# Optimization experiments

Measured on AMD Instinct MI355X. Metric: run time of the kernel, lower is better.

## Reference

```python
import jax, jax.numpy as jnp
import numpy as np

N = 50000      # nodes
E = 400000     # edges (before self-loops)
IN = 256       # in_dim
H = 4          # heads in layer 1
C = 64         # h_dim (per-head channels, layer 1)
OUT = 16       # out_dim (layer 2, 1 head)
NEG_SLOPE = 0.2


def gatv2_layer(x, src, dst, Wl, bl, Wr, br, att, bias, heads, ch, concat, num_nodes):
    # x: [N, F]; src/dst: [E']; Wl/Wr: [F, heads*ch]; att: [heads, ch]
    xl = (x @ Wl + bl).reshape(num_nodes, heads, ch)  # source transform
    xr = (x @ Wr + br).reshape(num_nodes, heads, ch)  # target transform
    m = xl[src] + xr[dst]                              # [E', H, C] gather
    e = jnp.sum(jax.nn.leaky_relu(m, NEG_SLOPE) * att, axis=-1)  # [E', H]
    # segment softmax over incoming edges of each dst node (self-loops ensure non-empty)
    emax = jax.ops.segment_max(e, dst, num_segments=num_nodes)   # [N, H]
    ee = jnp.exp(e - emax[dst])
    denom = jax.ops.segment_sum(ee, dst, num_segments=num_nodes)  # [N, H]
    alpha = ee / (denom[dst] + 1e-16)                              # [E', H]
    out = jax.ops.segment_sum(alpha[..., None] * xl[src], dst, num_segments=num_nodes)  # [N,H,C]
    if concat:
        out = out.reshape(num_nodes, heads * ch)
    else:
        out = out.mean(axis=1)
    return out + bias


def setup_inputs() -> dict:
    key = jax.random.key(0)
    ks = jax.random.split(key, 16)
    s = 0.05
    inp = {
        "x": jax.random.normal(ks[0], (N, IN), jnp.float32),
        "edge_index": jax.random.randint(ks[1], (2, E), 0, N),
        # layer 1 params (in_dim -> heads*h_dim)
        "Wl1": jax.random.normal(ks[2], (IN, H * C), jnp.float32) * s,
        "bl1": jnp.zeros((H * C,), jnp.float32),
        "Wr1": jax.random.normal(ks[3], (IN, H * C), jnp.float32) * s,
        "br1": jnp.zeros((H * C,), jnp.float32),
        "att1": jax.random.normal(ks[4], (H, C), jnp.float32) * s,
        "bias1": jnp.zeros((H * C,), jnp.float32),
        # layer 2 params (heads*h_dim -> out_dim, 1 head)
        "Wl2": jax.random.normal(ks[5], (H * C, OUT), jnp.float32) * s,
        "bl2": jnp.zeros((OUT,), jnp.float32),
        "Wr2": jax.random.normal(ks[6], (H * C, OUT), jnp.float32) * s,
        "br2": jnp.zeros((OUT,), jnp.float32),
        "att2": jax.random.normal(ks[7], (1, OUT), jnp.float32) * s,
        "bias2": jnp.zeros((OUT,), jnp.float32),
    }
    return inp


def reference(x, edge_index, Wl1, bl1, Wr1, br1, att1, bias1, Wl2, bl2, Wr2, br2, att2, bias2):
    # add self loops (PyG GATv2Conv default add_self_loops=True)
    loop = jnp.arange(N, dtype=edge_index.dtype)
    src = jnp.concatenate([edge_index[0], loop])
    dst = jnp.concatenate([edge_index[1], loop])
    h = gatv2_layer(x, src, dst, Wl1, bl1, Wr1, br1, att1, bias1, H, C, True, N)
    h = jnp.tanh(h)
    o = gatv2_layer(h, src, dst, Wl2, bl2, Wr2, br2, att2, bias2, 1, OUT, False, N)
    return o, jax.nn.log_softmax(o, axis=1)
```

## Files before the change

kernel.cpp:

```cpp
#include <hip/hip_runtime.h>

typedef __bf16 bfv8 __attribute__((ext_vector_type(8)));
typedef float f32x4 __attribute__((ext_vector_type(4)));
typedef short shortv8 __attribute__((ext_vector_type(8)));
typedef unsigned short usv8 __attribute__((ext_vector_type(8)));

__device__ __forceinline__ float b2f(unsigned short u) {
  unsigned int v = ((unsigned int)u) << 16;
  float f;
  __builtin_memcpy(&f, &v, 4);
  return f;
}
__device__ __forceinline__ unsigned short f2b(float f) {
  unsigned int u;
  __builtin_memcpy(&u, &f, 4);
  u += 0x7fffu + ((u >> 16) & 1u);
  return (unsigned short)(u >> 16);
}

__global__ void probe_kernel(const unsigned short* __restrict__ x, int* __restrict__ flag) {
  int lane = threadIdx.x;
  int cnt = 0;
  for (int i = lane; i < 4096; i += 64) {
    unsigned int e = (x[i] >> 7) & 0xffu;
    if (e >= 0x86u) cnt++;
  }
#pragma unroll
  for (int off = 1; off < 64; off <<= 1) cnt += __shfl_xor(cnt, off, 64);
  if (lane == 0) *flag = (cnt > 100) ? 1 : 0;
}

__global__ __launch_bounds__(256) void conv_x_kernel(const void* __restrict__ x,
                                                     unsigned short* __restrict__ dst,
                                                     const int* __restrict__ flagp, int n) {
  int i = (blockIdx.x * 256 + threadIdx.x) * 4;
  if (i >= n) return;
  if (*flagp) {
    float4 f = *reinterpret_cast<const float4*>((const float*)x + i);
    ushort4 o;
    o.x = f2b(f.x); o.y = f2b(f.y); o.z = f2b(f.z); o.w = f2b(f.w);
    *reinterpret_cast<ushort4*>(dst + i) = o;
  } else {
    *reinterpret_cast<ushort4*>(dst + i) =
        *reinterpret_cast<const ushort4*>((const unsigned short*)x + i);
  }
}

#define P_TOT 140352
__global__ __launch_bounds__(256) void conv_params_kernel(
    const void* p0, const void* p1, const void* p2, const void* p3,
    const void* p4, const void* p5, const void* p6, const void* p7,
    const void* p8, const void* p9, const void* p10, const void* p11,
    unsigned short* __restrict__ dst, const int* __restrict__ flagp) {
  int i = blockIdx.x * 256 + threadIdx.x;
  if (i >= P_TOT) return;
  const int offs[13] = {0, 65536, 65792, 131328, 131584, 131840, 132096,
                        136192, 136208, 140304, 140320, 140336, P_TOT};
  const void* ptrs[12] = {p0, p1, p2, p3, p4, p5, p6, p7, p8, p9, p10, p11};
  int flag = *flagp;
  int t = 0;
  while (i >= offs[t + 1]) t++;
  int local = i - offs[t];
  unsigned short v;
  if (flag) v = f2b(((const float*)ptrs[t])[local]);
  else v = ((const unsigned short*)ptrs[t])[local];
  dst[i] = v;
}

__global__ __launch_bounds__(256) void transpose_w_kernel(
    const unsigned short* __restrict__ Pc,
    unsigned short* __restrict__ WT1, unsigned short* __restrict__ WT2) {
  int idx = blockIdx.x * 256 + threadIdx.x;
  if (idx < 512 * 256) {
    int n = idx >> 8, k = idx & 255;
    WT1[idx] = (n < 256) ? Pc[0 + k * 256 + n]
                         : Pc[65792 + k * 256 + (n - 256)];
  } else {
    int j = idx - 512 * 256;
    if (j < 32 * 256) {
      int n = j >> 8, k = j & 255;
      WT2[j] = (n < 16) ? Pc[132096 + k * 16 + n]
                        : Pc[136208 + k * 16 + (n - 16)];
    }
  }
}

__global__ __launch_bounds__(256) void gemm1_kernel(
    const unsigned short* __restrict__ X,
    const unsigned short* __restrict__ WT,
    const unsigned short* __restrict__ bl, const unsigned short* __restrict__ br,
    unsigned short* __restrict__ C, int M) {
  __shared__ unsigned short smem[18432];
  const int t = threadIdx.x;
  const int lane = t & 63;
  const int w = t >> 6;
  const int quad = lane >> 4;
  const int l16 = lane & 15;
  const int n_blk = blockIdx.x;
  const int m_base = blockIdx.y * 128 + (w >> 1) * 64;
  const int n_base = n_blk * 128 + (w & 1) * 64;

  const int st_row = t >> 3;
  const int st_seg = t & 7;
  const unsigned short* wt_base =
      WT + ((size_t)(n_blk * 128 + st_row)) * 256 + st_seg * 8;

  f32x4 acc[4][4];
#pragma unroll
  for (int i = 0; i < 4; i++)
#pragma unroll
    for (int j = 0; j < 4; j++) acc[i][j] = (f32x4){0.f, 0.f, 0.f, 0.f};

  shortv8 st[4];
#pragma unroll
  for (int i = 0; i < 4; i++)
    st[i] = *reinterpret_cast<const shortv8*>(wt_base + (size_t)(32 * i) * 256);
#pragma unroll
  for (int i = 0; i < 4; i++) {
    int row = st_row + 32 * i;
    *reinterpret_cast<shortv8*>(smem + row * 64 + ((st_seg ^ (row & 7)) * 8)) = st[i];
  }
  __syncthreads();

#pragma unroll
  for (int c = 0; c < 4; c++) {
    if (c < 3) {
#pragma unroll
      for (int i = 0; i < 4; i++)
        st[i] = *reinterpret_cast<const shortv8*>(wt_base + (size_t)(32 * i) * 256 +
                                                  (c + 1) * 64);
    }
    const unsigned short* bb = smem + (c & 1) * 8192;
#pragma unroll
    for (int sub = 0; sub < 2; sub++) {
      bfv8 a[4], b[4];
      int seg_r = sub * 4 + quad;
#pragma unroll
      for (int i = 0; i < 4; i++) {
        int row = m_base + 16 * i + l16;
        if (row >= M) row = M - 1;
        a[i] = *reinterpret_cast<const bfv8*>(X + (size_t)row * 256 + c * 64 + sub * 32 +
                                              quad * 8);
      }
#pragma unroll
      for (int j = 0; j < 4; j++) {
        int col = (w & 1) * 64 + 16 * j + l16;
        b[j] = *reinterpret_cast<const bfv8*>(bb + col * 64 + ((seg_r ^ (col & 7)) * 8));
      }
#pragma unroll
      for (int i = 0; i < 4; i++)
#pragma unroll
        for (int j = 0; j < 4; j++)
          acc[i][j] = __builtin_amdgcn_mfma_f32_16x16x32_bf16(a[i], b[j], acc[i][j], 0, 0, 0);
    }
    if (c < 3) {
      int buf = (c + 1) & 1;
#pragma unroll
      for (int i = 0; i < 4; i++) {
        int row = st_row + 32 * i;
        *reinterpret_cast<shortv8*>(smem + buf * 8192 + row * 64 +
                                    ((st_seg ^ (row & 7)) * 8)) = st[i];
      }
      __syncthreads();
    }
  }

  __syncthreads();
  unsigned short* lt = smem + w * 4608;
#pragma unroll
  for (int j = 0; j < 4; j++) {
    int col = n_base + 16 * j + l16;
    float bias = (col < 256) ? b2f(bl[col]) : b2f(br[col - 256]);
#pragma unroll
    for (int i = 0; i < 4; i++)
#pragma unroll
      for (int r = 0; r < 4; r++)
        lt[(16 * i + quad * 4 + r) * 72 + 16 * j + l16] = f2b(acc[i][j][r] + bias);
  }
#pragma unroll
  for (int pass = 0; pass < 8; pass++) {
    int row = pass * 8 + (lane >> 3);
    int colg = (lane & 7) * 8;
    shortv8 v = *reinterpret_cast<const shortv8*>(lt + row * 72 + colg);
    int grow = m_base + row;
    if (grow < M)
      *reinterpret_cast<shortv8*>(C + (size_t)grow * 512 + n_base + colg) = v;
  }
}

__global__ __launch_bounds__(256) void gemm2_kernel(
    const unsigned short* __restrict__ H, const unsigned short* __restrict__ WT,
    const unsigned short* __restrict__ bl, const unsigned short* __restrict__ br,
    float* __restrict__ C, int M) {
  const int lane = threadIdx.x & 63;
  const int w = threadIdx.x >> 6;
  const int quad = lane >> 4;
  const int l16 = lane & 15;
  const int m_base = blockIdx.x * 256 + w * 64;

  f32x4 acc[4][2];
#pragma unroll
  for (int i = 0; i < 4; i++)
#pragma unroll
    for (int j = 0; j < 2; j++) acc[i][j] = (f32x4){0.f, 0.f, 0.f, 0.f};

#pragma unroll
  for (int k0 = 0; k0 < 256; k0 += 32) {
    bfv8 a[4], b[2];
#pragma unroll
    for (int i = 0; i < 4; i++) {
      int row = m_base + 16 * i + l16;
      if (row >= M) row = M - 1;
      a[i] = *reinterpret_cast<const bfv8*>(H + (size_t)row * 256 + k0 + quad * 8);
    }
#pragma unroll
    for (int j = 0; j < 2; j++) {
      int col = 16 * j + l16;
      b[j] = *reinterpret_cast<const bfv8*>(WT + (size_t)col * 256 + k0 + quad * 8);
    }
#pragma unroll
    for (int i = 0; i < 4; i++)
#pragma unroll
      for (int j = 0; j < 2; j++)
        acc[i][j] = __builtin_amdgcn_mfma_f32_16x16x32_bf16(a[i], b[j], acc[i][j], 0, 0, 0);
  }

#pragma unroll
  for (int j = 0; j < 2; j++) {
    int col = 16 * j + l16;
    float bias = (j == 0) ? b2f(bl[l16]) : b2f(br[l16]);
#pragma unroll
    for (int i = 0; i < 4; i++) {
#pragma unroll
      for (int r = 0; r < 4; r++) {
        int row = m_base + 16 * i + quad * 4 + r;
        if (row < M) C[(size_t)row * 32 + col] = acc[i][j][r] + bias;
      }
    }
  }
}

__global__ __launch_bounds__(256) void count_kernel(const int* __restrict__ ei, int E, int Nn,
                                                    int* __restrict__ cnt) {
  int i = blockIdx.x * 256 + threadIdx.x;
  int total = E + Nn;
  if (i >= total) return;
  int d = (i < E) ? ei[E + i] : (i - E);
  if ((unsigned)d >= (unsigned)Nn) d = 0;
  atomicAdd(&cnt[d], 1);
}

__global__ __launch_bounds__(1024) void scan1_kernel(const int* __restrict__ cnt,
                                                     int* __restrict__ row_start,
                                                     int* __restrict__ blkTot, int Nn) {
  __shared__ int buf[1024];
  int t = threadIdx.x;
  int i = blockIdx.x * 1024 + t;
  int v = (i < Nn) ? cnt[i] : 0;
  buf[t] = v;
  __syncthreads();
  for (int off = 1; off < 1024; off <<= 1) {
    int x = (t >= off) ? buf[t - off] : 0;
    __syncthreads();
    buf[t] += x;
    __syncthreads();
  }
  if (i < Nn) row_start[i] = buf[t] - v;
  if (t == 1023) blkTot[blockIdx.x] = buf[1023];
}

__global__ __launch_bounds__(64) void scan2_kernel(const int* __restrict__ blkTot,
                                                   int* __restrict__ blkOff, int nb,
                                                   int* __restrict__ row_start, int Nn,
                                                   int total) {
  int lane = threadIdx.x;
  int v = (lane < nb) ? blkTot[lane] : 0;
  int s = v;
#pragma unroll
  for (int off = 1; off < 64; off <<= 1) {
    int u = __shfl_up(s, off, 64);
    if (lane >= off) s += u;
  }
  if (lane < nb) blkOff[lane] = s - v;
  if (lane == 0) row_start[Nn] = total;
}

__global__ __launch_bounds__(1024) void scan3_kernel(int* __restrict__ row_start,
                                                     int* __restrict__ cursor,
                                                     const int* __restrict__ blkOff, int Nn) {
  int i = blockIdx.x * 1024 + threadIdx.x;
  if (i < Nn) {
    int val = row_start[i] + blkOff[blockIdx.x];
    row_start[i] = val;
    cursor[i] = val;
  }
}

__global__ __launch_bounds__(256) void fill_kernel(const int* __restrict__ ei, int E, int Nn,
                                                   int* __restrict__ cursor,
                                                   int* __restrict__ csr_src) {
  int i = blockIdx.x * 256 + threadIdx.x;
  int total = E + Nn;
  if (i >= total) return;
  int s, d;
  if (i < E) { s = ei[i]; d = ei[E + i]; } else { s = i - E; d = i - E; }
  if ((unsigned)d >= (unsigned)Nn) d = 0;
  if ((unsigned)s >= (unsigned)Nn) s = 0;
  int pos = atomicAdd(&cursor[d], 1);
  if ((unsigned)pos < (unsigned)total) csr_src[pos] = s;
}

__global__ __launch_bounds__(256) void agg1_kernel(
    const unsigned short* __restrict__ C1,
    const unsigned short* __restrict__ att1,
    const unsigned short* __restrict__ bias1,
    const int* __restrict__ row_start, const int* __restrict__ csr_src,
    unsigned short* __restrict__ H1,
    int Nn, int Etot) {
  int wid = blockIdx.x * 4 + (threadIdx.x >> 6);
  if (wid >= Nn) return;
  int lane = threadIdx.x & 63;
  int half = lane >> 5;
  int c0 = (lane & 31) * 8;

  float at[8], xr[8];
  {
    usv8 a8 = *reinterpret_cast<const usv8*>(att1 + c0);
    usv8 r8 = *reinterpret_cast<const usv8*>(C1 + (size_t)wid * 512 + 256 + c0);
#pragma unroll
    for (int k = 0; k < 8; k++) { at[k] = b2f(a8[k]); xr[k] = b2f(r8[k]); }
  }

  float denom = 0.f;
  float acc[8] = {0.f, 0.f, 0.f, 0.f, 0.f, 0.f, 0.f, 0.f};
  int beg = row_start[wid], end = row_start[wid + 1];
  if (beg < 0) beg = 0;
  if (end < beg || end - beg > Etot) end = beg;

#pragma unroll 2
  for (int i = beg; i < end; i += 2) {
    int p = i + half;
    bool valid = p < end;
    int pc = valid ? p : i;
    int s = csr_src[pc];
    if ((unsigned)s >= (unsigned)Nn) s = 0;
    usv8 row = *reinterpret_cast<const usv8*>(C1 + (size_t)s * 512 + c0);
    float xl[8], dot = 0.f;
#pragma unroll
    for (int k = 0; k < 8; k++) {
      xl[k] = b2f(row[k]);
      float m = xl[k] + xr[k];
      float l = fmaxf(m, 0.2f * m);
      dot = fmaf(l, at[k], dot);
    }
    dot += __shfl_xor(dot, 1, 64);
    dot += __shfl_xor(dot, 2, 64);
    dot += __shfl_xor(dot, 4, 64);
    dot = fminf(fmaxf(dot, -60.f), 60.f);
    float wgt = valid ? __expf(dot) : 0.f;
    denom += wgt;
#pragma unroll
    for (int k = 0; k < 8; k++) acc[k] = fmaf(wgt, xl[k], acc[k]);
  }
  denom += __shfl_xor(denom, 32, 64);
#pragma unroll
  for (int k = 0; k < 8; k++) acc[k] += __shfl_xor(acc[k], 32, 64);

  if (half == 0) {
    float inv = 1.f / (denom + 1e-16f);
    usv8 b8 = *reinterpret_cast<const usv8*>(bias1 + c0);
    usv8 o8;
#pragma unroll
    for (int k = 0; k < 8; k++) {
      float x = acc[k] * inv + b2f(b8[k]);
      float e2 = __expf(2.f * x);
      float th = (e2 - 1.f) / (e2 + 1.f);
      if (!(th == th)) th = 0.f;
      o8[k] = f2b(th);
    }
    *reinterpret_cast<usv8*>(H1 + (size_t)wid * 256 + c0) = o8;
  }
}

__global__ __launch_bounds__(256) void agg2_kernel(
    const float* __restrict__ C2,
    const unsigned short* __restrict__ att2,
    const unsigned short* __restrict__ bias2,
    const int* __restrict__ row_start, const int* __restrict__ csr_src,
    float* __restrict__ out,
    int Nn, int Etot) {
  int wid = blockIdx.x * 4 + (threadIdx.x >> 6);
  if (wid >= Nn) return;
  int lane = threadIdx.x & 63;
  int eslot = lane >> 2;
  int cg = (lane & 3) * 4;

  float at[4], xr[4];
  {
    ushort4 a4 = *reinterpret_cast<const ushort4*>(att2 + cg);
    at[0] = b2f(a4.x); at[1] = b2f(a4.y); at[2] = b2f(a4.z); at[3] = b2f(a4.w);
    float4 r4 = *reinterpret_cast<const float4*>(C2 + (size_t)wid * 32 + 16 + cg);
    xr[0] = r4.x; xr[1] = r4.y; xr[2] = r4.z; xr[3] = r4.w;
  }

  float denom = 0.f;
  float acc[4] = {0.f, 0.f, 0.f, 0.f};
  int beg = row_start[wid], end = row_start[wid + 1];
  if (beg < 0) beg = 0;
  if (end < beg || end - beg > Etot) end = beg;

  for (int i = beg; i < end; i += 16) {
    int p = i + eslot;
    bool valid = p < end;
    int pc = valid ? p : i;
    int s = csr_src[pc];
    if ((unsigned)s >= (unsigned)Nn) s = 0;
    float4 x4 = *reinterpret_cast<const float4*>(C2 + (size_t)s * 32 + cg);
    float xl[4] = {x4.x, x4.y, x4.z, x4.w};
    float dot = 0.f;
#pragma unroll
    for (int k = 0; k < 4; k++) {
      float m = xl[k] + xr[k];
      float l = fmaxf(m, 0.2f * m);
      dot = fmaf(l, at[k], dot);
    }
    dot += __shfl_xor(dot, 1, 64);
    dot += __shfl_xor(dot, 2, 64);
    dot = fminf(fmaxf(dot, -60.f), 60.f);
    float wgt = valid ? __expf(dot) : 0.f;
    denom += wgt;
#pragma unroll
    for (int k = 0; k < 4; k++) acc[k] = fmaf(wgt, xl[k], acc[k]);
  }
#pragma unroll
  for (int off = 4; off <= 32; off <<= 1) {
    denom += __shfl_xor(denom, off, 64);
#pragma unroll
    for (int k = 0; k < 4; k++) acc[k] += __shfl_xor(acc[k], off, 64);
  }

  float inv = 1.f / (denom + 1e-16f);
  ushort4 b4 = *reinterpret_cast<const ushort4*>(bias2 + cg);
  float bb[4] = {b2f(b4.x), b2f(b4.y), b2f(b4.z), b2f(b4.w)};
  float o[4];
#pragma unroll
  for (int k = 0; k < 4; k++) {
    o[k] = acc[k] * inv + bb[k];
    if (!(o[k] == o[k])) o[k] = 0.f;
  }
  float mx = fmaxf(fmaxf(o[0], o[1]), fmaxf(o[2], o[3]));
  mx = fmaxf(mx, __shfl_xor(mx, 1, 64));
  mx = fmaxf(mx, __shfl_xor(mx, 2, 64));
  float se = 0.f;
#pragma unroll
  for (int k = 0; k < 4; k++) se += __expf(o[k] - mx);
  se += __shfl_xor(se, 1, 64);
  se += __shfl_xor(se, 2, 64);
  float ls = logf(se);
  if (lane < 4) {
    float4 vo = {o[0], o[1], o[2], o[3]};
    float4 vl = {o[0] - mx - ls, o[1] - mx - ls, o[2] - mx - ls, o[3] - mx - ls};
    *reinterpret_cast<float4*>(out + (size_t)wid * 16 + cg) = vo;
    *reinterpret_cast<float4*>(out + (size_t)Nn * 16 + (size_t)wid * 16 + cg) = vl;
  }
}

extern "C" void kernel_launch(void* const* d_in, const int* in_sizes, int n_in,
                              void* d_out, int out_size, void* d_ws, size_t ws_size,
                              hipStream_t stream) {
  const void* x_raw = d_in[0];
  const int* ei     = (const int*)d_in[1];

  const int M = in_sizes[0] / 256;
  const int E = in_sizes[1] / 2;
  const int TOT = E + M;
  const int NX = M * 256;

  char* ws = (char*)d_ws;
  size_t off = 0;
  auto alloc = [&](size_t bytes) -> void* {
    void* p = ws + off;
    off = (off + bytes + 255) & ~(size_t)255;
    return p;
  };
  int*            flag   = (int*)alloc(4);
  unsigned short* Pc     = (unsigned short*)alloc((size_t)P_TOT * 2);
  unsigned short* Xc     = (unsigned short*)alloc((size_t)NX * 2);
  unsigned short* WT1    = (unsigned short*)alloc((size_t)512 * 256 * 2);
  unsigned short* WT2    = (unsigned short*)alloc((size_t)32 * 256 * 2);
  int*            cnt    = (int*)alloc((size_t)M * 4);
  int*            cursor = (int*)alloc((size_t)M * 4);
  int*            row_start = (int*)alloc((size_t)(M + 1) * 4);
  int*            csr_src   = (int*)alloc((size_t)TOT * 4);
  int*            blkTot = (int*)alloc(64 * 4);
  int*            blkOff = (int*)alloc(64 * 4);
  float*          C2     = (float*)alloc((size_t)M * 32 * 4);
  unsigned short* C1     = (unsigned short*)alloc((size_t)M * 512 * 2);
  const size_t need = off;
  (void)n_in;
  unsigned short* H1 = Xc;

  if (ws_size < need) {
    hipMemsetAsync(d_out, 0, (size_t)out_size * 4, stream);
    return;
  }

  unsigned short* bl1c   = Pc + 65536;
  unsigned short* br1c   = Pc + 131328;
  unsigned short* att1c  = Pc + 131584;
  unsigned short* bias1c = Pc + 131840;
  unsigned short* bl2c   = Pc + 136192;
  unsigned short* br2c   = Pc + 140304;
  unsigned short* att2c  = Pc + 140320;
  unsigned short* bias2c = Pc + 140336;

  hipMemsetAsync(cnt, 0, (size_t)M * 4, stream);

  probe_kernel<<<1, 64, 0, stream>>>((const unsigned short*)x_raw, flag);
  conv_x_kernel<<<(NX / 4 + 255) / 256, 256, 0, stream>>>(x_raw, Xc, flag, NX);
  conv_params_kernel<<<(P_TOT + 255) / 256, 256, 0, stream>>>(
      d_in[2], d_in[3], d_in[4], d_in[5], d_in[6], d_in[7], d_in[8], d_in[9],
      d_in[10], d_in[11], d_in[12], d_in[13], Pc, flag);

  transpose_w_kernel<<<(512 * 256 + 32 * 256 + 255) / 256, 256, 0, stream>>>(Pc, WT1, WT2);

  dim3 g1(4, (M + 127) / 128);
  gemm1_kernel<<<g1, 256, 0, stream>>>(Xc, WT1, bl1c, br1c, C1, M);

  count_kernel<<<(TOT + 255) / 256, 256, 0, stream>>>(ei, E, M, cnt);
  int nb = (M + 1023) / 1024;
  scan1_kernel<<<nb, 1024, 0, stream>>>(cnt, row_start, blkTot, M);
  scan2_kernel<<<1, 64, 0, stream>>>(blkTot, blkOff, nb, row_start, M, TOT);
  scan3_kernel<<<nb, 1024, 0, stream>>>(row_start, cursor, blkOff, M);
  fill_kernel<<<(TOT + 255) / 256, 256, 0, stream>>>(ei, E, M, cursor, csr_src);

  agg1_kernel<<<(M + 3) / 4, 256, 0, stream>>>(C1, att1c, bias1c, row_start, csr_src,
                                               H1, M, TOT);

  gemm2_kernel<<<(M + 255) / 256, 256, 0, stream>>>(H1, WT2, bl2c, br2c, C2, M);

  agg2_kernel<<<(M + 3) / 4, 256, 0, stream>>>(C2, att2c, bias2c, row_start, csr_src,
                                               (float*)d_out, M, TOT);
}
```

Before: 304.2 us.

## Batch-prefetch CSR indices per wave, use DPP reductions and packed math in aggregation

Both aggregation kernels now load up to 64 CSR source indices at once, one per lane, and hand them out with wave shuffles instead of a dependent global load on every edge iteration. Cross-lane reductions that used __shfl_xor are replaced with DPP moves. The layer-1 math moves to packed f32x2 with faster bf16 unpacking, and tanh and the reciprocal use rcp approximations. The aim is shorter latency chains per edge and fewer LDS-backed shuffles, at the cost of slightly lower precision in the reciprocal and tanh.

```diff
diff --git a/kernel.cpp b/kernel.cpp
--- a/kernel.cpp
+++ b/kernel.cpp
@@ -2,6 +2,7 @@
 
 typedef __bf16 bfv8 __attribute__((ext_vector_type(8)));
 typedef float f32x4 __attribute__((ext_vector_type(4)));
+typedef float f32x2 __attribute__((ext_vector_type(2)));
 typedef short shortv8 __attribute__((ext_vector_type(8)));
 typedef unsigned short usv8 __attribute__((ext_vector_type(8)));
 
@@ -16,6 +17,28 @@
   __builtin_memcpy(&u, &f, 4);
   u += 0x7fffu + ((u >> 16) & 1u);
   return (unsigned short)(u >> 16);
+}
+
+__device__ __forceinline__ f32x2 bf2x(unsigned int u) {
+  f32x2 r;
+  r.x = __builtin_bit_cast(float, u << 16);
+  r.y = __builtin_bit_cast(float, u & 0xffff0000u);
+  return r;
+}
+
+template <int CTRL>
+__device__ __forceinline__ float dpp_mv(float x) {
+  int xi = __builtin_bit_cast(int, x);
+  int yi = __builtin_amdgcn_update_dpp(0, xi, CTRL, 0xf, 0xf, true);
+  return __builtin_bit_cast(float, yi);
+}
+
+__device__ __forceinline__ float tanh_fast(float x) {
+  float e2 = __expf(2.f * x);
+  float r = __builtin_amdgcn_rcpf(e2 + 1.f);
+  float th = fmaf(-2.f, r, 1.f);
+  if (!(th == th)) th = 0.f;
+  return th;
 }
 
 __global__ void probe_kernel(const unsigned short* __restrict__ x, int* __restrict__ flag) {
@@ -323,62 +346,78 @@
   int half = lane >> 5;
   int c0 = (lane & 31) * 8;
 
-  float at[8], xr[8];
+  f32x2 at2[4], xr2[4];
   {
-    usv8 a8 = *reinterpret_cast<const usv8*>(att1 + c0);
-    usv8 r8 = *reinterpret_cast<const usv8*>(C1 + (size_t)wid * 512 + 256 + c0);
-#pragma unroll
-    for (int k = 0; k < 8; k++) { at[k] = b2f(a8[k]); xr[k] = b2f(r8[k]); }
+    uint4 a4 = *reinterpret_cast<const uint4*>(att1 + c0);
+    uint4 r4 = *reinterpret_cast<const uint4*>(C1 + (size_t)wid * 512 + 256 + c0);
+    at2[0] = bf2x(a4.x); at2[1] = bf2x(a4.y); at2[2] = bf2x(a4.z); at2[3] = bf2x(a4.w);
+    xr2[0] = bf2x(r4.x); xr2[1] = bf2x(r4.y); xr2[2] = bf2x(r4.z); xr2[3] = bf2x(r4.w);
   }
 
   float denom = 0.f;
-  float acc[8] = {0.f, 0.f, 0.f, 0.f, 0.f, 0.f, 0.f, 0.f};
+  f32x2 acc2[4] = {};
   int beg = row_start[wid], end = row_start[wid + 1];
   if (beg < 0) beg = 0;
   if (end < beg || end - beg > Etot) end = beg;
 
+  for (int base = beg; base < end; base += 64) {
+    int cend = min(end, base + 64);
+    int pl = base + lane;
+    if (pl >= end) pl = end - 1;
+    int s_pre = csr_src[pl];
 #pragma unroll 2
-  for (int i = beg; i < end; i += 2) {
-    int p = i + half;
-    bool valid = p < end;
-    int pc = valid ? p : i;
-    int s = csr_src[pc];
-    if ((unsigned)s >= (unsigned)Nn) s = 0;
-    usv8 row = *reinterpret_cast<const usv8*>(C1 + (size_t)s * 512 + c0);
-    float xl[8], dot = 0.f;
-#pragma unroll
-    for (int k = 0; k < 8; k++) {
-      xl[k] = b2f(row[k]);
-      float m = xl[k] + xr[k];
-      float l = fmaxf(m, 0.2f * m);
-      dot = fmaf(l, at[k], dot);
-    }
-    dot += __shfl_xor(dot, 1, 64);
-    dot += __shfl_xor(dot, 2, 64);
-    dot += __shfl_xor(dot, 4, 64);
-    dot = fminf(fmaxf(dot, -60.f), 60.f);
-    float wgt = valid ? __expf(dot) : 0.f;
-    denom += wgt;
-#pragma unroll
-    for (int k = 0; k < 8; k++) acc[k] = fmaf(wgt, xl[k], acc[k]);
+    for (int i = base; i < cend; i += 2) {
+      int p = i + half;
+      bool valid = p < cend;
+      int s = __shfl(s_pre, p - base, 64);
+      if ((unsigned)s >= (unsigned)Nn) s = 0;
+      uint4 rw = *reinterpret_cast<const uint4*>(C1 + (size_t)s * 512 + c0);
+      f32x2 xl0 = bf2x(rw.x), xl1 = bf2x(rw.y), xl2 = bf2x(rw.z), xl3 = bf2x(rw.w);
+      f32x2 m0 = xl0 + xr2[0], m1 = xl1 + xr2[1];
+      f32x2 m2 = xl2 + xr2[2], m3 = xl3 + xr2[3];
+      f32x2 l0 = __builtin_elementwise_max(m0, m0 * 0.2f);
+      f32x2 l1 = __builtin_elementwise_max(m1, m1 * 0.2f);
+      f32x2 l2 = __builtin_elementwise_max(m2, m2 * 0.2f);
+      f32x2 l3 = __builtin_elementwise_max(m3, m3 * 0.2f);
+      f32x2 d2 = l0 * at2[0];
+      d2 += l1 * at2[1];
+      d2 += l2 * at2[2];
+      d2 += l3 * at2[3];
+      float dot = d2.x + d2.y;
+      dot += dpp_mv<0xB1>(dot);
+      dot += dpp_mv<0x4E>(dot);
+      dot += dpp_mv<0x141>(dot);
+      dot = fminf(fmaxf(dot, -60.f), 60.f);
+      float wgt = valid ? __expf(dot) : 0.f;
+      denom += wgt;
+      acc2[0] += xl0 * wgt;
+      acc2[1] += xl1 * wgt;
+      acc2[2] += xl2 * wgt;
+      acc2[3] += xl3 * wgt;
+    }
   }
   denom += __shfl_xor(denom, 32, 64);
 #pragma unroll
-  for (int k = 0; k < 8; k++) acc[k] += __shfl_xor(acc[k], 32, 64);
+  for (int k = 0; k < 4; k++) {
+    acc2[k].x += __shfl_xor(acc2[k].x, 32, 64);
+    acc2[k].y += __shfl_xor(acc2[k].y, 32, 64);
+  }
 
   if (half == 0) {
-    float inv = 1.f / (denom + 1e-16f);
-    usv8 b8 = *reinterpret_cast<const usv8*>(bias1 + c0);
-    usv8 o8;
-#pragma unroll
-    for (int k = 0; k < 8; k++) {
-      float x = acc[k] * inv + b2f(b8[k]);
-      float e2 = __expf(2.f * x);
-      float th = (e2 - 1.f) / (e2 + 1.f);
-      if (!(th == th)) th = 0.f;
-      o8[k] = f2b(th);
-    }
-    *reinterpret_cast<usv8*>(H1 + (size_t)wid * 256 + c0) = o8;
+    float inv = __builtin_amdgcn_rcpf(denom + 1e-16f);
+    uint4 b4 = *reinterpret_cast<const uint4*>(bias1 + c0);
+    f32x2 bb[4] = {bf2x(b4.x), bf2x(b4.y), bf2x(b4.z), bf2x(b4.w)};
+    uint4 o;
+    unsigned int od[4];
+#pragma unroll
+    for (int k = 0; k < 4; k++) {
+      f32x2 xv = acc2[k] * inv + bb[k];
+      float t0 = tanh_fast(xv.x);
+      float t1 = tanh_fast(xv.y);
+      od[k] = (unsigned int)f2b(t0) | ((unsigned int)f2b(t1) << 16);
+    }
+    o.x = od[0]; o.y = od[1]; o.z = od[2]; o.w = od[3];
+    *reinterpret_cast<uint4*>(H1 + (size_t)wid * 256 + c0) = o;
   }
 }
 
@@ -409,37 +448,49 @@
   if (beg < 0) beg = 0;
   if (end < beg || end - beg > Etot) end = beg;
 
-  for (int i = beg; i < end; i += 16) {
-    int p = i + eslot;
-    bool valid = p < end;
-    int pc = valid ? p : i;
-    int s = csr_src[pc];
-    if ((unsigned)s >= (unsigned)Nn) s = 0;
-    float4 x4 = *reinterpret_cast<const float4*>(C2 + (size_t)s * 32 + cg);
-    float xl[4] = {x4.x, x4.y, x4.z, x4.w};
-    float dot = 0.f;
-#pragma unroll
-    for (int k = 0; k < 4; k++) {
-      float m = xl[k] + xr[k];
-      float l = fmaxf(m, 0.2f * m);
-      dot = fmaf(l, at[k], dot);
-    }
-    dot += __shfl_xor(dot, 1, 64);
-    dot += __shfl_xor(dot, 2, 64);
-    dot = fminf(fmaxf(dot, -60.f), 60.f);
-    float wgt = valid ? __expf(dot) : 0.f;
-    denom += wgt;
-#pragma unroll
-    for (int k = 0; k < 4; k++) acc[k] = fmaf(wgt, xl[k], acc[k]);
-  }
-#pragma unroll
-  for (int off = 4; off <= 32; off <<= 1) {
+  for (int base = beg; base < end; base += 64) {
+    int cend = min(end, base + 64);
+    int pl = base + lane;
+    if (pl >= end) pl = end - 1;
+    int s_pre = csr_src[pl];
+    for (int i = base; i < cend; i += 16) {
+      int p = i + eslot;
+      bool valid = p < cend;
+      int s = __shfl(s_pre, p - base, 64);
+      if ((unsigned)s >= (unsigned)Nn) s = 0;
+      float4 x4 = *reinterpret_cast<const float4*>(C2 + (size_t)s * 32 + cg);
+      float xl[4] = {x4.x, x4.y, x4.z, x4.w};
+      float dot = 0.f;
+#pragma unroll
+      for (int k = 0; k < 4; k++) {
+        float m = xl[k] + xr[k];
+        float l = fmaxf(m, 0.2f * m);
+        dot = fmaf(l, at[k], dot);
+      }
+      dot += dpp_mv<0xB1>(dot);
+      dot += dpp_mv<0x4E>(dot);
+      dot = fminf(fmaxf(dot, -60.f), 60.f);
+      float wgt = valid ? __expf(dot) : 0.f;
+      denom += wgt;
+#pragma unroll
+      for (int k = 0; k < 4; k++) acc[k] = fmaf(wgt, xl[k], acc[k]);
+    }
+  }
+  denom += dpp_mv<0x124>(denom);
+  denom += dpp_mv<0x128>(denom);
+#pragma unroll
+  for (int k = 0; k < 4; k++) {
+    acc[k] += dpp_mv<0x124>(acc[k]);
+    acc[k] += dpp_mv<0x128>(acc[k]);
+  }
+#pragma unroll
+  for (int off = 16; off <= 32; off <<= 1) {
     denom += __shfl_xor(denom, off, 64);
 #pragma unroll
     for (int k = 0; k < 4; k++) acc[k] += __shfl_xor(acc[k], off, 64);
   }
 
-  float inv = 1.f / (denom + 1e-16f);
+  float inv = __builtin_amdgcn_rcpf(denom + 1e-16f);
   ushort4 b4 = *reinterpret_cast<const ushort4*>(bias2 + cg);
   float bb[4] = {b2f(b4.x), b2f(b4.y), b2f(b4.z), b2f(b4.w)};
   float o[4];
@@ -449,13 +500,13 @@
     if (!(o[k] == o[k])) o[k] = 0.f;
   }
   float mx = fmaxf(fmaxf(o[0], o[1]), fmaxf(o[2], o[3]));
-  mx = fmaxf(mx, __shfl_xor(mx, 1, 64));
-  mx = fmaxf(mx, __shfl_xor(mx, 2, 64));
+  mx = fmaxf(mx, dpp_mv<0xB1>(mx));
+  mx = fmaxf(mx, dpp_mv<0x4E>(mx));
   float se = 0.f;
 #pragma unroll
   for (int k = 0; k < 4; k++) se += __expf(o[k] - mx);
-  se += __shfl_xor(se, 1, 64);
-  se += __shfl_xor(se, 2, 64);
+  se += dpp_mv<0xB1>(se);
+  se += dpp_mv<0x4E>(se);
   float ls = logf(se);
   if (lane < 4) {
     float4 vo = {o[0], o[1], o[2], o[3]};
```

Measured after the change: 293.3 us. 1.04x faster.
